# Performance work log

Hardware: AMD Instinct MI355X
Metric: run time of the kernel (lower is better)

Reference implementation:

```python
import jax, jax.numpy as jnp
import numpy as np

EMB = 1024
CTX = 32
F_IN, R, F_OUT = 1024, 16, 1024
N_EXP = 16
H1 = 2048   # expert / gating hidden
H2 = 512    # expert output width
B = 8


def _init(key, shape, fan_in):
    return jax.random.normal(key, shape, dtype=jnp.float32) / np.sqrt(fan_in)


def setup_inputs() -> dict:
    key = jax.random.key(0)
    ks = jax.random.split(key, 14)
    return {
        "s": jax.random.normal(ks[0], (B, EMB), dtype=jnp.float32),
        # gating: Linear(EMB,2048) -> ReLU -> Linear(2048,N_EXP) -> Softmax
        "Wg1": _init(ks[1], (EMB, H1), EMB),
        "bg1": jnp.zeros((H1,), jnp.float32),
        "Wg2": _init(ks[2], (H1, N_EXP), H1),
        "bg2": jnp.zeros((N_EXP,), jnp.float32),
        # experts (stacked): Linear(EMB+CTX,2048) -> ReLU -> Linear(2048,512)
        "W1": _init(ks[3], (N_EXP, EMB + CTX, H1), EMB + CTX),
        "b1": jnp.zeros((N_EXP, H1), jnp.float32),
        "W2": _init(ks[4], (N_EXP, H1, H2), H1),
        "b2": jnp.zeros((N_EXP, H2), jnp.float32),
        # decoders
        "WA": _init(ks[5], (H2, F_IN * R), H2),
        "bA": jnp.zeros((F_IN * R,), jnp.float32),
        "WB": _init(ks[6], (H2, R * F_OUT), H2),
        "bB": jnp.zeros((R * F_OUT,), jnp.float32),
    }


def reference(s, Wg1, bg1, Wg2, bg2, W1, b1, W2, b2, WA, bA, WB, bB):
    # gating weights over experts: [B, E]
    weights = jax.nn.softmax(jax.nn.relu(s @ Wg1 + bg1) @ Wg2 + bg2, axis=-1)

    # Expert layer-1. Input is concat([s, one_hot(c)]); since the context part
    # is a one-hot, its contribution is just a row of the context block of W1.
    W1s = W1[:, :EMB, :]              # [E, EMB, H1]
    W1c = W1[:, EMB:, :]              # [E, CTX, H1]
    base = jnp.einsum('bi,eih->ebh', s, W1s) + b1[:, None, :]   # [E, B, H1]
    # h[c,e,b,:] = relu(base[e,b,:] + W1c[e,c,:])
    h = jax.nn.relu(base[None] + jnp.transpose(W1c, (1, 0, 2))[:, :, None, :])  # [C,E,B,H1]

    # Expert layer-2: [C, E, B, H2]
    eo = jnp.einsum('cebh,ehd->cebd', h, W2) + b2[None, :, None, :]

    # softmax-weighted mixture over experts: [C, B, H2]
    z = jnp.einsum('be,cebd->cbd', weights, eo)

    A = (z @ WA + bA).reshape(CTX, B, F_IN, R)
    Bm = (z @ WB + bB).reshape(CTX, B, R, F_OUT)
    return A, Bm
```

## Files before the change

kernel.cpp:

```cpp
#include <hip/hip_runtime.h>
#include <hip/hip_bf16.h>

#define EMB 1024
#define CTX 32
#define NEXP 16
#define H1 2048
#define H2 512
#define NBIG 16384

typedef __attribute__((ext_vector_type(8))) short short8;
typedef __attribute__((ext_vector_type(4))) float floatx4;

__device__ inline unsigned short bf_bits(float x) {
  unsigned u = __builtin_bit_cast(unsigned, x);
  u += 0x7fffu + ((u >> 16) & 1u);
  return (unsigned short)(u >> 16);
}
__device__ inline unsigned pk_bf16(float a, float b) {
  return (unsigned)bf_bits(a) | ((unsigned)bf_bits(b) << 16);
}

__global__ void __launch_bounds__(256) k_gate1(const float* __restrict__ s,
                                               const float* __restrict__ Wg1,
                                               const float* __restrict__ bg1,
                                               float* __restrict__ g1) {
  __shared__ float red[16][16][8];
  int t = threadIdx.x;
  int c = t & 15, kk = t >> 4;
  int h = blockIdx.x * 16 + c;
  float acc[8];
#pragma unroll
  for (int b = 0; b < 8; ++b) acc[b] = 0.f;
  int k0 = kk * 64;
  for (int k = k0; k < k0 + 64; ++k) {
    float w = Wg1[(size_t)k * H1 + h];
#pragma unroll
    for (int b = 0; b < 8; ++b) acc[b] += s[b * EMB + k] * w;
  }
#pragma unroll
  for (int b = 0; b < 8; ++b) red[kk][c][b] = acc[b];
  __syncthreads();
  if (t < 128) {
    int cc = t >> 3, b = t & 7;
    float v = 0.f;
#pragma unroll
    for (int q = 0; q < 16; ++q) v += red[q][cc][b];
    int hh = blockIdx.x * 16 + cc;
    v += bg1[hh];
    g1[b * H1 + hh] = fmaxf(v, 0.f);
  }
}

__global__ void __launch_bounds__(256) k_gate2(const float* __restrict__ g1,
                                               const float* __restrict__ Wg2,
                                               const float* __restrict__ bg2,
                                               float* __restrict__ logits) {
  __shared__ float red[256][8];
  int e = blockIdx.x, t = threadIdx.x;
  int k0 = t * 8;
  float wv[8];
#pragma unroll
  for (int j = 0; j < 8; ++j) wv[j] = Wg2[(size_t)(k0 + j) * NEXP + e];
  float acc[8];
#pragma unroll
  for (int b = 0; b < 8; ++b) {
    float4 ga = *(const float4*)&g1[b * H1 + k0];
    float4 gb = *(const float4*)&g1[b * H1 + k0 + 4];
    acc[b] = ga.x * wv[0] + ga.y * wv[1] + ga.z * wv[2] + ga.w * wv[3] +
             gb.x * wv[4] + gb.y * wv[5] + gb.z * wv[6] + gb.w * wv[7];
  }
#pragma unroll
  for (int b = 0; b < 8; ++b) red[t][b] = acc[b];
  __syncthreads();
  for (int off = 128; off > 0; off >>= 1) {
    if (t < off) {
#pragma unroll
      for (int b = 0; b < 8; ++b) red[t][b] += red[t + off][b];
    }
    __syncthreads();
  }
  if (t < 8) logits[t * NEXP + e] = red[0][t] + bg2[e];
}

__global__ void __launch_bounds__(512) k_base(const float* __restrict__ s,
                                              const float* __restrict__ W1,
                                              const float* __restrict__ b1,
                                              float* __restrict__ base) {
  __shared__ float sl[8 * EMB];
  __shared__ float red[8][64][17];
  int t = threadIdx.x;
  int ht = blockIdx.x;
  int e = blockIdx.y;
#pragma unroll
  for (int i = 0; i < 4; ++i) {
    int idx = (t + i * 512) * 4;
    *(float4*)&sl[idx] = *(const float4*)&s[idx];
  }
  __syncthreads();
  int hp = t & 63;
  int kk = t >> 6;
  int h = ht * 128 + hp * 2;
  const float* wp = W1 + (size_t)e * 1056 * H1 + h;
  float a0[8], a1[8];
#pragma unroll
  for (int b = 0; b < 8; ++b) { a0[b] = 0.f; a1[b] = 0.f; }
  int k0 = kk * 128;
  for (int k = k0; k < k0 + 128; ++k) {
    float2 w = *(const float2*)(wp + (size_t)k * H1);
#pragma unroll
    for (int b = 0; b < 8; ++b) {
      float sv = sl[b * EMB + k];
      a0[b] += sv * w.x;
      a1[b] += sv * w.y;
    }
  }
#pragma unroll
  for (int b = 0; b < 8; ++b) {
    red[kk][hp][b * 2] = a0[b];
    red[kk][hp][b * 2 + 1] = a1[b];
  }
  __syncthreads();
  if (t < 64) {
    int hh = ht * 128 + t * 2;
#pragma unroll
    for (int b = 0; b < 8; ++b) {
      float v0 = 0.f, v1 = 0.f;
#pragma unroll
      for (int q = 0; q < 8; ++q) {
        v0 += red[q][t][b * 2];
        v1 += red[q][t][b * 2 + 1];
      }
      float2 bv = *(const float2*)&b1[e * H1 + hh];
      float2 o;
      o.x = v0 + bv.x;
      o.y = v1 + bv.y;
      *(float2*)&base[(size_t)(e * 8 + b) * H1 + hh] = o;
    }
  }
}

__global__ void __launch_bounds__(256) k_expert(const float* __restrict__ base,
                                                const float* __restrict__ W1,
                                                const float* __restrict__ W2,
                                                float* __restrict__ eo) {
  __shared__ __align__(16) unsigned short hl[64 * 64];
  int dt = blockIdx.x, mt = blockIdx.y, e = blockIdx.z;
  int t = threadIdx.x;
  int lane = t & 63, w = t >> 6;
  int fr = lane & 15, quad = lane >> 4;
  int d = dt * 64 + w * 16 + fr;

  const float* baseE = base + (size_t)e * 8 * H1;
  const float* w1cE = W1 + (size_t)e * 1056 * H1 + (size_t)EMB * H1;
  const float* w2E = W2 + (size_t)e * H1 * H2;

  int fm = lane;
  int fb = fm & 7;
  int fc = mt * 8 + (fm >> 3);
  int fkp = w * 16;
  const float* bsrc = baseE + (size_t)fb * H1 + fkp;
  const float* csrc = w1cE + (size_t)fc * H1 + fkp;
  int xr = fm & 7;
  unsigned short* wp0 = &hl[fm * 64 + (((2 * w) ^ xr) * 8)];
  unsigned short* wp1 = &hl[fm * 64 + (((2 * w + 1) ^ xr) * 8)];

  floatx4 zero4 = {0.f, 0.f, 0.f, 0.f};
  floatx4 acc[4];
#pragma unroll
  for (int r = 0; r < 4; ++r) acc[r] = zero4;

  float4 rb[4], rc[4];
#pragma unroll
  for (int j = 0; j < 4; ++j) {
    rb[j] = *(const float4*)(bsrc + j * 4);
    rc[j] = *(const float4*)(csrc + j * 4);
  }

  for (int k0 = 0; k0 < H1; k0 += 64) {
    float hv[16];
#pragma unroll
    for (int j = 0; j < 4; ++j) {
      hv[j * 4 + 0] = fmaxf(rb[j].x + rc[j].x, 0.f);
      hv[j * 4 + 1] = fmaxf(rb[j].y + rc[j].y, 0.f);
      hv[j * 4 + 2] = fmaxf(rb[j].z + rc[j].z, 0.f);
      hv[j * 4 + 3] = fmaxf(rb[j].w + rc[j].w, 0.f);
    }
    union { short8 v; unsigned u[4]; } p0, p1;
#pragma unroll
    for (int j = 0; j < 4; ++j) {
      p0.u[j] = pk_bf16(hv[2 * j], hv[2 * j + 1]);
      p1.u[j] = pk_bf16(hv[8 + 2 * j], hv[8 + 2 * j + 1]);
    }
    __syncthreads();
    *(short8*)wp0 = p0.v;
    *(short8*)wp1 = p1.v;
    __syncthreads();
    if (k0 + 64 < H1) {
#pragma unroll
      for (int j = 0; j < 4; ++j) {
        rb[j] = *(const float4*)(bsrc + k0 + 64 + j * 4);
        rc[j] = *(const float4*)(csrc + k0 + 64 + j * 4);
      }
    }
#pragma unroll
    for (int ks = 0; ks < 2; ++ks) {
      const float* wq = w2E + (size_t)(k0 + ks * 32 + quad * 8) * H2 + d;
      float f0 = wq[0], f1 = wq[H2], f2 = wq[2 * H2], f3 = wq[3 * H2];
      float f4 = wq[4 * H2], f5 = wq[5 * H2], f6 = wq[6 * H2], f7 = wq[7 * H2];
      union { short8 v; unsigned u[4]; } bp;
      bp.u[0] = pk_bf16(f0, f1);
      bp.u[1] = pk_bf16(f2, f3);
      bp.u[2] = pk_bf16(f4, f5);
      bp.u[3] = pk_bf16(f6, f7);
#pragma unroll
      for (int rt = 0; rt < 4; ++rt) {
        int m = rt * 16 + fr;
        short8 av = *(const short8*)&hl[m * 64 + (((ks * 4 + quad) ^ (m & 7)) * 8)];
        acc[rt] = __builtin_amdgcn_mfma_f32_16x16x32_bf16(av, bp.v, acc[rt], 0, 0, 0);
      }
    }
  }
#pragma unroll
  for (int rt = 0; rt < 4; ++rt) {
#pragma unroll
    for (int i = 0; i < 4; ++i) {
      int gm = mt * 64 + rt * 16 + quad * 4 + i;
      int cc = gm >> 3, bb = gm & 7;
      eo[(((size_t)cc * NEXP + e) * 8 + bb) * H2 + d] = acc[rt][i];
    }
  }
}

__global__ void __launch_bounds__(256) k_mix(const float* __restrict__ eo,
                                             const float* __restrict__ logits,
                                             const float* __restrict__ b2,
                                             unsigned short* __restrict__ zbf) {
  int dt = blockIdx.x;
  int c = blockIdx.y;
  int t = threadIdx.x;
  int d = dt * 64 + (t & 63);
  int bq = t >> 6;
#pragma unroll
  for (int bi = 0; bi < 2; ++bi) {
    int b = bq + bi * 4;
    float lg[16];
    float mx = -1e30f;
#pragma unroll
    for (int e2 = 0; e2 < 16; ++e2) {
      lg[e2] = logits[b * NEXP + e2];
      mx = fmaxf(mx, lg[e2]);
    }
    float sum = 0.f;
#pragma unroll
    for (int e2 = 0; e2 < 16; ++e2) {
      lg[e2] = __expf(lg[e2] - mx);
      sum += lg[e2];
    }
    float inv = 1.f / sum;
    float acc = 0.f;
#pragma unroll
    for (int e2 = 0; e2 < 16; ++e2) {
      float v = eo[(((size_t)c * NEXP + e2) * 8 + b) * H2 + d] + b2[e2 * H2 + d];
      acc += lg[e2] * v;
    }
    acc *= inv;
    zbf[((size_t)c * 8 + b) * H2 + d] = bf_bits(acc);
  }
}

__global__ void __launch_bounds__(256) k_lora(const unsigned short* __restrict__ zbf,
                                              const float* __restrict__ WA,
                                              const float* __restrict__ bA,
                                              const float* __restrict__ WB,
                                              const float* __restrict__ bB,
                                              float* __restrict__ out) {
  int nb = blockIdx.x, mt = blockIdx.y, ms = blockIdx.z;
  const float* W = ms ? WB : WA;
  const float* bias = ms ? bB : bA;
  float* o = out + (size_t)ms * 4194304;
  int t = threadIdx.x;
  int lane = t & 63, w = t >> 6;
  int fr = lane & 15, quad = lane >> 4;
  int m0 = mt * 128;
  int n0 = nb * 128 + w * 32;

  floatx4 zero4 = {0.f, 0.f, 0.f, 0.f};
  floatx4 acc[8][2];
#pragma unroll
  for (int r = 0; r < 8; ++r) {
    acc[r][0] = zero4;
    acc[r][1] = zero4;
  }
  for (int k0 = 0; k0 < H2; k0 += 32) {
    short8 af[8];
#pragma unroll
    for (int rt = 0; rt < 8; ++rt) {
      int m = m0 + rt * 16 + fr;
      af[rt] = *(const short8*)&zbf[(size_t)m * H2 + k0 + quad * 8];
    }
#pragma unroll
    for (int nt = 0; nt < 2; ++nt) {
      int n = n0 + nt * 16 + fr;
      const float* wq = W + (size_t)(k0 + quad * 8) * NBIG + n;
      float f0 = wq[0], f1 = wq[NBIG], f2 = wq[2 * NBIG], f3 = wq[3 * NBIG];
      float f4 = wq[4 * NBIG], f5 = wq[5 * NBIG], f6 = wq[6 * NBIG], f7 = wq[7 * NBIG];
      union { short8 v; unsigned u[4]; } bp;
      bp.u[0] = pk_bf16(f0, f1);
      bp.u[1] = pk_bf16(f2, f3);
      bp.u[2] = pk_bf16(f4, f5);
      bp.u[3] = pk_bf16(f6, f7);
#pragma unroll
      for (int rt = 0; rt < 8; ++rt)
        acc[rt][nt] = __builtin_amdgcn_mfma_f32_16x16x32_bf16(af[rt], bp.v, acc[rt][nt], 0, 0, 0);
    }
  }
#pragma unroll
  for (int nt = 0; nt < 2; ++nt) {
    int n = n0 + nt * 16 + fr;
    float bv = bias[n];
#pragma unroll
    for (int rt = 0; rt < 8; ++rt) {
#pragma unroll
      for (int i = 0; i < 4; ++i) {
        int m = m0 + rt * 16 + quad * 4 + i;
        o[(size_t)m * NBIG + n] = acc[rt][nt][i] + bv;
      }
    }
  }
}

extern "C" void kernel_launch(void* const* d_in, const int* in_sizes, int n_in,
                              void* d_out, int out_size, void* d_ws, size_t ws_size,
                              hipStream_t stream) {
  const float* s = (const float*)d_in[0];
  const float* Wg1 = (const float*)d_in[1];
  const float* bg1 = (const float*)d_in[2];
  const float* Wg2 = (const float*)d_in[3];
  const float* bg2 = (const float*)d_in[4];
  const float* W1 = (const float*)d_in[5];
  const float* b1 = (const float*)d_in[6];
  const float* W2 = (const float*)d_in[7];
  const float* b2 = (const float*)d_in[8];
  const float* WA = (const float*)d_in[9];
  const float* bA = (const float*)d_in[10];
  const float* WB = (const float*)d_in[11];
  const float* bB = (const float*)d_in[12];
  float* out = (float*)d_out;

  char* ws = (char*)d_ws;
  float* g1 = (float*)(ws);
  float* logits = (float*)(ws + 65536);
  float* base = (float*)(ws + 131072);
  float* eo = (float*)(ws + 131072 + 1048576);
  unsigned short* zbf = (unsigned short*)(ws + 131072 + 1048576 + 8388608);

  k_gate1<<<128, 256, 0, stream>>>(s, Wg1, bg1, g1);
  k_gate2<<<16, 256, 0, stream>>>(g1, Wg2, bg2, logits);
  k_base<<<dim3(16, 16), 512, 0, stream>>>(s, W1, b1, base);
  k_expert<<<dim3(8, 4, 16), 256, 0, stream>>>(base, W1, W2, eo);
  k_mix<<<dim3(8, 32), 256, 0, stream>>>(eo, logits, b2, zbf);
  k_lora<<<dim3(128, 2, 2), 256, 0, stream>>>(zbf, WA, bA, WB, bB, out);
}
```

Measured before the change: 429.4 us.

## Pre-pack weights to transposed bf16 and split expert GEMM with K-split

Adds a transpose-and-convert kernel that packs W2, WA and WB into K-contiguous bf16 copies on every call, so the GEMM kernels can load B fragments as single 16-byte vectors instead of eight strided fp32 loads plus conversion. The expert stage is split into a kernel that materialises the ReLU hidden activations in bf16 and a GEMM that splits K in two, writing partial results that k_mix then sums. The LoRA GEMM is retiled to 64-wide N tiles over the transposed weights. The cost is extra passes over the weights each call and more workspace traffic.

```diff
diff --git a/kernel.cpp b/kernel.cpp
--- a/kernel.cpp
+++ b/kernel.cpp
@@ -139,99 +139,95 @@
   }
 }
 
-__global__ void __launch_bounds__(256) k_expert(const float* __restrict__ base,
-                                                const float* __restrict__ W1,
-                                                const float* __restrict__ W2,
-                                                float* __restrict__ eo) {
-  __shared__ __align__(16) unsigned short hl[64 * 64];
-  int dt = blockIdx.x, mt = blockIdx.y, e = blockIdx.z;
+__global__ void __launch_bounds__(256) k_packT(const float* __restrict__ src,
+                                               unsigned short* __restrict__ dst,
+                                               int K, int N, long bstride) {
+  __shared__ float tl[64][65];
+  const float* S = src + (size_t)blockIdx.z * bstride;
+  unsigned short* D = dst + (size_t)blockIdx.z * bstride;
+  int nt = blockIdx.x, kt = blockIdx.y, t = threadIdx.x;
+  int r = t >> 4, c4 = (t & 15) * 4;
+#pragma unroll
+  for (int i = 0; i < 4; ++i) {
+    int row = r + i * 16;
+    float4 v = *(const float4*)&S[(size_t)(kt * 64 + row) * N + nt * 64 + c4];
+    *(float4*)&tl[row][c4] = v;
+  }
+  __syncthreads();
+#pragma unroll
+  for (int j = 0; j < 2; ++j) {
+    int nl = (t >> 3) + j * 32;
+    int k8 = (t & 7) * 8;
+    union { short8 v; unsigned u[4]; } p;
+#pragma unroll
+    for (int q = 0; q < 4; ++q)
+      p.u[q] = pk_bf16(tl[k8 + 2 * q][nl], tl[k8 + 2 * q + 1][nl]);
+    *(short8*)&D[(size_t)(nt * 64 + nl) * K + kt * 64 + k8] = p.v;
+  }
+}
+
+__global__ void __launch_bounds__(256) k_h(const float* __restrict__ base,
+                                           const float* __restrict__ W1,
+                                           unsigned short* __restrict__ h) {
+  int c = blockIdx.x, e = blockIdx.y;
   int t = threadIdx.x;
-  int lane = t & 63, w = t >> 6;
+  int b = t >> 5, l = t & 31;
+  const float* bp = base + ((size_t)e * 8 + b) * H1;
+  const float* cp = W1 + (size_t)e * 1056 * H1 + (size_t)EMB * H1 + (size_t)c * H1;
+  unsigned short* hp = h + ((size_t)e * 256 + c * 8 + b) * H1;
+#pragma unroll
+  for (int kc = 0; kc < 8; ++kc) {
+    int k = kc * 256 + l * 8;
+    float4 x0 = *(const float4*)&bp[k];
+    float4 x1 = *(const float4*)&bp[k + 4];
+    float4 y0 = *(const float4*)&cp[k];
+    float4 y1 = *(const float4*)&cp[k + 4];
+    union { short8 v; unsigned u[4]; } p;
+    p.u[0] = pk_bf16(fmaxf(x0.x + y0.x, 0.f), fmaxf(x0.y + y0.y, 0.f));
+    p.u[1] = pk_bf16(fmaxf(x0.z + y0.z, 0.f), fmaxf(x0.w + y0.w, 0.f));
+    p.u[2] = pk_bf16(fmaxf(x1.x + y1.x, 0.f), fmaxf(x1.y + y1.y, 0.f));
+    p.u[3] = pk_bf16(fmaxf(x1.z + y1.z, 0.f), fmaxf(x1.w + y1.w, 0.f));
+    *(short8*)&hp[k] = p.v;
+  }
+}
+
+__global__ void __launch_bounds__(256) k_egemm(const unsigned short* __restrict__ h,
+                                               const unsigned short* __restrict__ W2T,
+                                               float* __restrict__ eo2) {
+  int dt = blockIdx.x;
+  int mk = blockIdx.y;
+  int e = blockIdx.z;
+  int mt = mk & 3, ks = mk >> 2;
+  int t = threadIdx.x, lane = t & 63, w = t >> 6;
   int fr = lane & 15, quad = lane >> 4;
-  int d = dt * 64 + w * 16 + fr;
-
-  const float* baseE = base + (size_t)e * 8 * H1;
-  const float* w1cE = W1 + (size_t)e * 1056 * H1 + (size_t)EMB * H1;
-  const float* w2E = W2 + (size_t)e * H1 * H2;
-
-  int fm = lane;
-  int fb = fm & 7;
-  int fc = mt * 8 + (fm >> 3);
-  int fkp = w * 16;
-  const float* bsrc = baseE + (size_t)fb * H1 + fkp;
-  const float* csrc = w1cE + (size_t)fc * H1 + fkp;
-  int xr = fm & 7;
-  unsigned short* wp0 = &hl[fm * 64 + (((2 * w) ^ xr) * 8)];
-  unsigned short* wp1 = &hl[fm * 64 + (((2 * w + 1) ^ xr) * 8)];
-
+  int n = dt * 64 + w * 16 + fr;
+  const unsigned short* hA = h + ((size_t)e * 256 + mt * 64 + fr) * H1 + ks * 1024 + quad * 8;
+  const unsigned short* bB = W2T + ((size_t)e * H2 + n) * H1 + ks * 1024 + quad * 8;
   floatx4 zero4 = {0.f, 0.f, 0.f, 0.f};
   floatx4 acc[4];
 #pragma unroll
   for (int r = 0; r < 4; ++r) acc[r] = zero4;
-
-  float4 rb[4], rc[4];
-#pragma unroll
-  for (int j = 0; j < 4; ++j) {
-    rb[j] = *(const float4*)(bsrc + j * 4);
-    rc[j] = *(const float4*)(csrc + j * 4);
-  }
-
-  for (int k0 = 0; k0 < H1; k0 += 64) {
-    float hv[16];
-#pragma unroll
-    for (int j = 0; j < 4; ++j) {
-      hv[j * 4 + 0] = fmaxf(rb[j].x + rc[j].x, 0.f);
-      hv[j * 4 + 1] = fmaxf(rb[j].y + rc[j].y, 0.f);
-      hv[j * 4 + 2] = fmaxf(rb[j].z + rc[j].z, 0.f);
-      hv[j * 4 + 3] = fmaxf(rb[j].w + rc[j].w, 0.f);
-    }
-    union { short8 v; unsigned u[4]; } p0, p1;
-#pragma unroll
-    for (int j = 0; j < 4; ++j) {
-      p0.u[j] = pk_bf16(hv[2 * j], hv[2 * j + 1]);
-      p1.u[j] = pk_bf16(hv[8 + 2 * j], hv[8 + 2 * j + 1]);
-    }
-    __syncthreads();
-    *(short8*)wp0 = p0.v;
-    *(short8*)wp1 = p1.v;
-    __syncthreads();
-    if (k0 + 64 < H1) {
-#pragma unroll
-      for (int j = 0; j < 4; ++j) {
-        rb[j] = *(const float4*)(bsrc + k0 + 64 + j * 4);
-        rc[j] = *(const float4*)(csrc + k0 + 64 + j * 4);
-      }
-    }
-#pragma unroll
-    for (int ks = 0; ks < 2; ++ks) {
-      const float* wq = w2E + (size_t)(k0 + ks * 32 + quad * 8) * H2 + d;
-      float f0 = wq[0], f1 = wq[H2], f2 = wq[2 * H2], f3 = wq[3 * H2];
-      float f4 = wq[4 * H2], f5 = wq[5 * H2], f6 = wq[6 * H2], f7 = wq[7 * H2];
-      union { short8 v; unsigned u[4]; } bp;
-      bp.u[0] = pk_bf16(f0, f1);
-      bp.u[1] = pk_bf16(f2, f3);
-      bp.u[2] = pk_bf16(f4, f5);
-      bp.u[3] = pk_bf16(f6, f7);
-#pragma unroll
-      for (int rt = 0; rt < 4; ++rt) {
-        int m = rt * 16 + fr;
-        short8 av = *(const short8*)&hl[m * 64 + (((ks * 4 + quad) ^ (m & 7)) * 8)];
-        acc[rt] = __builtin_amdgcn_mfma_f32_16x16x32_bf16(av, bp.v, acc[rt], 0, 0, 0);
-      }
-    }
-  }
+#pragma unroll 2
+  for (int k0 = 0; k0 < 1024; k0 += 32) {
+    short8 bf = *(const short8*)&bB[k0];
+#pragma unroll
+    for (int rt = 0; rt < 4; ++rt) {
+      short8 af = *(const short8*)&hA[(size_t)rt * 16 * H1 + k0];
+      acc[rt] = __builtin_amdgcn_mfma_f32_16x16x32_bf16(af, bf, acc[rt], 0, 0, 0);
+    }
+  }
+  float* op = eo2 + (size_t)ks * 2097152;
 #pragma unroll
   for (int rt = 0; rt < 4; ++rt) {
 #pragma unroll
     for (int i = 0; i < 4; ++i) {
       int gm = mt * 64 + rt * 16 + quad * 4 + i;
-      int cc = gm >> 3, bb = gm & 7;
-      eo[(((size_t)cc * NEXP + e) * 8 + bb) * H2 + d] = acc[rt][i];
-    }
-  }
-}
-
-__global__ void __launch_bounds__(256) k_mix(const float* __restrict__ eo,
+      op[(((size_t)(gm >> 3) * NEXP + e) * 8 + (gm & 7)) * H2 + n] = acc[rt][i];
+    }
+  }
+}
+
+__global__ void __launch_bounds__(256) k_mix(const float* __restrict__ eo2,
                                              const float* __restrict__ logits,
                                              const float* __restrict__ b2,
                                              unsigned short* __restrict__ zbf) {
@@ -260,7 +256,8 @@
     float acc = 0.f;
 #pragma unroll
     for (int e2 = 0; e2 < 16; ++e2) {
-      float v = eo[(((size_t)c * NEXP + e2) * 8 + b) * H2 + d] + b2[e2 * H2 + d];
+      size_t idx = (((size_t)c * NEXP + e2) * 8 + b) * H2 + d;
+      float v = eo2[idx] + eo2[idx + 2097152] + b2[e2 * H2 + d];
       acc += lg[e2] * v;
     }
     acc *= inv;
@@ -269,62 +266,41 @@
 }
 
 __global__ void __launch_bounds__(256) k_lora(const unsigned short* __restrict__ zbf,
-                                              const float* __restrict__ WA,
+                                              const unsigned short* __restrict__ WAT,
                                               const float* __restrict__ bA,
-                                              const float* __restrict__ WB,
+                                              const unsigned short* __restrict__ WBT,
                                               const float* __restrict__ bB,
                                               float* __restrict__ out) {
-  int nb = blockIdx.x, mt = blockIdx.y, ms = blockIdx.z;
-  const float* W = ms ? WB : WA;
+  int nt = blockIdx.x, mt = blockIdx.y, ms = blockIdx.z;
+  const unsigned short* WT = ms ? WBT : WAT;
   const float* bias = ms ? bB : bA;
   float* o = out + (size_t)ms * 4194304;
-  int t = threadIdx.x;
-  int lane = t & 63, w = t >> 6;
+  int t = threadIdx.x, lane = t & 63, w = t >> 6;
   int fr = lane & 15, quad = lane >> 4;
+  int n = nt * 64 + w * 16 + fr;
   int m0 = mt * 128;
-  int n0 = nb * 128 + w * 32;
-
+  const unsigned short* A = zbf + ((size_t)m0 + fr) * H2 + quad * 8;
+  const unsigned short* B = WT + (size_t)n * H2 + quad * 8;
   floatx4 zero4 = {0.f, 0.f, 0.f, 0.f};
-  floatx4 acc[8][2];
-#pragma unroll
-  for (int r = 0; r < 8; ++r) {
-    acc[r][0] = zero4;
-    acc[r][1] = zero4;
-  }
+  floatx4 acc[8];
+#pragma unroll
+  for (int r = 0; r < 8; ++r) acc[r] = zero4;
+#pragma unroll 2
   for (int k0 = 0; k0 < H2; k0 += 32) {
-    short8 af[8];
+    short8 bf = *(const short8*)&B[k0];
 #pragma unroll
     for (int rt = 0; rt < 8; ++rt) {
-      int m = m0 + rt * 16 + fr;
-      af[rt] = *(const short8*)&zbf[(size_t)m * H2 + k0 + quad * 8];
-    }
-#pragma unroll
-    for (int nt = 0; nt < 2; ++nt) {
-      int n = n0 + nt * 16 + fr;
-      const float* wq = W + (size_t)(k0 + quad * 8) * NBIG + n;
-      float f0 = wq[0], f1 = wq[NBIG], f2 = wq[2 * NBIG], f3 = wq[3 * NBIG];
-      float f4 = wq[4 * NBIG], f5 = wq[5 * NBIG], f6 = wq[6 * NBIG], f7 = wq[7 * NBIG];
-      union { short8 v; unsigned u[4]; } bp;
-      bp.u[0] = pk_bf16(f0, f1);
-      bp.u[1] = pk_bf16(f2, f3);
-      bp.u[2] = pk_bf16(f4, f5);
-      bp.u[3] = pk_bf16(f6, f7);
-#pragma unroll
-      for (int rt = 0; rt < 8; ++rt)
-        acc[rt][nt] = __builtin_amdgcn_mfma_f32_16x16x32_bf16(af[rt], bp.v, acc[rt][nt], 0, 0, 0);
-    }
-  }
-#pragma unroll
-  for (int nt = 0; nt < 2; ++nt) {
-    int n = n0 + nt * 16 + fr;
-    float bv = bias[n];
-#pragma unroll
-    for (int rt = 0; rt < 8; ++rt) {
-#pragma unroll
-      for (int i = 0; i < 4; ++i) {
-        int m = m0 + rt * 16 + quad * 4 + i;
-        o[(size_t)m * NBIG + n] = acc[rt][nt][i] + bv;
-      }
+      short8 af = *(const short8*)&A[(size_t)rt * 16 * H2 + k0];
+      acc[rt] = __builtin_amdgcn_mfma_f32_16x16x32_bf16(af, bf, acc[rt], 0, 0, 0);
+    }
+  }
+  float bv = bias[n];
+#pragma unroll
+  for (int rt = 0; rt < 8; ++rt) {
+#pragma unroll
+    for (int i = 0; i < 4; ++i) {
+      int m = m0 + rt * 16 + quad * 4 + i;
+      o[(size_t)m * NBIG + n] = acc[rt][i] + bv;
     }
   }
 }
@@ -351,13 +327,21 @@
   float* g1 = (float*)(ws);
   float* logits = (float*)(ws + 65536);
   float* base = (float*)(ws + 131072);
-  float* eo = (float*)(ws + 131072 + 1048576);
-  unsigned short* zbf = (unsigned short*)(ws + 131072 + 1048576 + 8388608);
+  unsigned short* h = (unsigned short*)(ws + 1179648);
+  float* eo2 = (float*)(ws + 17956864);
+  unsigned short* zbf = (unsigned short*)(ws + 34734080);
+  unsigned short* W2T = (unsigned short*)(ws + 34996224);
+  unsigned short* WAT = (unsigned short*)(ws + 68550656);
+  unsigned short* WBT = (unsigned short*)(ws + 85327872);
 
   k_gate1<<<128, 256, 0, stream>>>(s, Wg1, bg1, g1);
   k_gate2<<<16, 256, 0, stream>>>(g1, Wg2, bg2, logits);
+  k_packT<<<dim3(8, 32, 16), 256, 0, stream>>>(W2, W2T, H1, H2, (long)H1 * H2);
+  k_packT<<<dim3(256, 8, 1), 256, 0, stream>>>(WA, WAT, H2, NBIG, 0);
+  k_packT<<<dim3(256, 8, 1), 256, 0, stream>>>(WB, WBT, H2, NBIG, 0);
   k_base<<<dim3(16, 16), 512, 0, stream>>>(s, W1, b1, base);
-  k_expert<<<dim3(8, 4, 16), 256, 0, stream>>>(base, W1, W2, eo);
-  k_mix<<<dim3(8, 32), 256, 0, stream>>>(eo, logits, b2, zbf);
-  k_lora<<<dim3(128, 2, 2), 256, 0, stream>>>(zbf, WA, bA, WB, bB, out);
-}
+  k_h<<<dim3(32, 16), 256, 0, stream>>>(base, W1, h);
+  k_egemm<<<dim3(8, 8, 16), 256, 0, stream>>>(h, W2T, eo2);
+  k_mix<<<dim3(8, 32), 256, 0, stream>>>(eo2, logits, b2, zbf);
+  k_lora<<<dim3(256, 2, 2), 256, 0, stream>>>(zbf, WAT, bA, WBT, bB, out);
+}
```

Result: slower. 504.0 us (+17.4%).
